# Kernel optimization log

Hardware: AMD Instinct MI355X
Metric: run time of the kernel (lower is better)

The kernel has to match this reference:

```python
import jax, jax.numpy as jnp
import numpy as np
from jax import lax

D_VOCAB = 262
D_EMB = 128
CONV_W = 5
PAD = CONV_W // 2  # 2


def setup_inputs() -> dict:
    key = jax.random.key(0)
    k1, k2, k3, k4, k5 = jax.random.split(key, 5)
    B, W, C = 128, 256, 16
    input = jax.random.randint(k1, (B, W, C), 0, D_VOCAB, dtype=jnp.int64)
    lengths = jax.random.randint(k2, (B, W), 1, C + 1, dtype=jnp.int64)
    # torch init: Embedding weight ~ N(0,1) then *0.1
    emb_weight = jax.random.normal(k3, (D_VOCAB, D_EMB), dtype=jnp.float32) * 0.1
    fan_in = D_EMB * CONV_W
    bound = 1.0 / np.sqrt(fan_in)
    conv_w = jax.random.uniform(k4, (D_EMB, D_EMB, CONV_W), dtype=jnp.float32, minval=-bound, maxval=bound)
    conv_b = jax.random.uniform(k5, (D_EMB,), dtype=jnp.float32, minval=-bound, maxval=bound)
    return {"input": input, "lengths": lengths, "emb_weight": emb_weight,
            "conv_w": conv_w, "conv_b": conv_b}


def reference(input, lengths, emb_weight, conv_w, conv_b):
    B, W, C = input.shape
    ids = input.reshape(B * W, C)                      # [N, C]
    embed = emb_weight[ids]                            # [N, C, E] gather
    x = jnp.transpose(embed, (0, 2, 1))                # [N, E, C] (NCW)
    y = lax.conv_general_dilated(
        x, conv_w,
        window_strides=(1,), padding=[(PAD, PAD)],
        dimension_numbers=("NCH", "OIH", "NCH"))       # [N, E, C]
    y = y + conv_b[None, :, None]
    out = jnp.max(y, axis=-1)                          # max-pool over chars
    return out.reshape(B, W, -1)                       # [B, W, E]
```

## Files before the change

### kernel.cpp

```cpp
#include <hip/hip_runtime.h>
#include <hip/hip_fp16.h>

#define D_VOCAB 262
#define D_EMB   128
#define KW      5
#define NCHAR   16
#define NKO     (KW * D_EMB)

typedef _Float16 h8 __attribute__((ext_vector_type(8)));
typedef float    f8 __attribute__((ext_vector_type(8)));


__global__ __launch_bounds__(256) void transpose_w_kernel(
    const float* __restrict__ cw, float* __restrict__ Wt2) {
  const int gid = blockIdx.x * 256 + threadIdx.x;
  const float val = cw[gid];
  const int o = gid / 640;
  const int r = gid - o * 640;
  const int i = r / 5;
  const int k = r - i * 5;
  Wt2[i * NKO + k * D_EMB + o] = val;
}

__global__ __launch_bounds__(128) void compute_P_kernel(
    const float* __restrict__ emb, const float* __restrict__ Wt2,
    __half* __restrict__ P) {
  __shared__ float emb_s[D_EMB];
  const int b = blockIdx.x;
  const int v = b / KW;
  const int k = b - v * KW;
  const int t = threadIdx.x;
  emb_s[t] = emb[v * D_EMB + t];
  __syncthreads();

  const float* col = Wt2 + k * D_EMB + t;
  float acc = 0.f;
#pragma unroll 16
  for (int i = 0; i < D_EMB; ++i) {
    acc += emb_s[i] * col[i * NKO];
  }
  P[v * NKO + k * D_EMB + t] = __float2half(acc);
}

__global__ __launch_bounds__(256) void conv_char_main_kernel(
    const int* __restrict__ ids, const _Float16* __restrict__ P,
    const float* __restrict__ bias, float* __restrict__ out) {
  const int lane = threadIdx.x & 63;
  const int wave = threadIdx.x >> 6;
  const int n_base = (blockIdx.x * 4 + wave) * 4;
  const int g4 = lane & 48;
  const int s = lane & 15;
  const int o = s * 8;
  const int n = n_base + (lane >> 4);

  const int myid = ids[n_base * NCHAR + lane];

  h8 win[5];
#pragma unroll
  for (int w = 0; w < 5; ++w) win[w] = (h8)(_Float16)0.f;
  h8 vmax = (h8)(_Float16)(-60000.f);

#pragma unroll
  for (int j = 0; j < NCHAR; ++j) {
    const int id = __shfl(myid, g4 + j);
    const _Float16* row = P + (size_t)id * NKO + o;
#pragma unroll
    for (int k = 0; k < KW; ++k) {
      const int c = j + 2 - k;
      if (c >= 0 && c < NCHAR) {
        const h8 val = *(const h8*)(row + k * D_EMB);
        win[c % 5] += val;
      }
    }
    if (j >= 2) {
      const int w = (j - 2) % 5;
      vmax = __builtin_elementwise_max(vmax, win[w]);
      win[w] = (h8)(_Float16)0.f;
    }
  }
  vmax = __builtin_elementwise_max(vmax, win[14 % 5]);
  vmax = __builtin_elementwise_max(vmax, win[15 % 5]);

  const f8 fv = __builtin_convertvector(vmax, f8);
  const f8 bv = *(const f8*)(bias + o);
  const f8 r = fv + bv;
  *(f8*)(out + (size_t)n * D_EMB + o) = r;
}

extern "C" void kernel_launch(void* const* d_in, const int* in_sizes, int n_in,
                              void* d_out, int out_size, void* d_ws, size_t ws_size,
                              hipStream_t stream) {
  const int*   input = (const int*)d_in[0];
  const float* emb   = (const float*)d_in[2];
  const float* cw    = (const float*)d_in[3];
  const float* cb    = (const float*)d_in[4];
  float* out = (float*)d_out;

  _Float16* P   = (_Float16*)d_ws;
  float*    Wt2 = (float*)((char*)d_ws + 335872);

  const int n_seq = in_sizes[0] / NCHAR;

  transpose_w_kernel<<<320, 256, 0, stream>>>(cw, Wt2);
  compute_P_kernel<<<D_VOCAB * KW, 128, 0, stream>>>(emb, Wt2, (__half*)P);

  const int blocks = n_seq / 16;
  conv_char_main_kernel<<<blocks, 256, 0, stream>>>(input, P, cb, out);
}
```

Baseline: 95.04 us.

## Map one wavefront per sequence with scalar id loads and half2 lanes

```diff
diff --git a/kernel.cpp b/kernel.cpp
--- a/kernel.cpp
+++ b/kernel.cpp
@@ -7,8 +7,8 @@
 #define NCHAR   16
 #define NKO     (KW * D_EMB)
 
+typedef _Float16 h2 __attribute__((ext_vector_type(2)));
 typedef _Float16 h8 __attribute__((ext_vector_type(8)));
-typedef float    f8 __attribute__((ext_vector_type(8)));
 
 
 __global__ __launch_bounds__(256) void transpose_w_kernel(
@@ -46,45 +46,43 @@
     const int* __restrict__ ids, const _Float16* __restrict__ P,
     const float* __restrict__ bias, float* __restrict__ out) {
   const int lane = threadIdx.x & 63;
-  const int wave = threadIdx.x >> 6;
-  const int n_base = (blockIdx.x * 4 + wave) * 4;
-  const int g4 = lane & 48;
-  const int s = lane & 15;
-  const int o = s * 8;
-  const int n = n_base + (lane >> 4);
+  int n = (int)((blockIdx.x * 256 + threadIdx.x) >> 6);
+  n = __builtin_amdgcn_readfirstlane(n);
 
-  const int myid = ids[n_base * NCHAR + lane];
+  const int* idrow = ids + n * NCHAR;
+  const int o = lane * 2;
 
-  h8 win[5];
+  h2 win[5];
 #pragma unroll
-  for (int w = 0; w < 5; ++w) win[w] = (h8)(_Float16)0.f;
-  h8 vmax = (h8)(_Float16)(-60000.f);
+  for (int w = 0; w < 5; ++w) win[w] = (h2)(_Float16)0.f;
+  h2 vmax = (h2)(_Float16)(-60000.f);
 
 #pragma unroll
   for (int j = 0; j < NCHAR; ++j) {
-    const int id = __shfl(myid, g4 + j);
+    const int id = idrow[j];
     const _Float16* row = P + (size_t)id * NKO + o;
 #pragma unroll
     for (int k = 0; k < KW; ++k) {
       const int c = j + 2 - k;
       if (c >= 0 && c < NCHAR) {
-        const h8 val = *(const h8*)(row + k * D_EMB);
+        const h2 val = *(const h2*)(row + k * D_EMB);
         win[c % 5] += val;
       }
     }
     if (j >= 2) {
       const int w = (j - 2) % 5;
       vmax = __builtin_elementwise_max(vmax, win[w]);
-      win[w] = (h8)(_Float16)0.f;
+      win[w] = (h2)(_Float16)0.f;
     }
   }
   vmax = __builtin_elementwise_max(vmax, win[14 % 5]);
   vmax = __builtin_elementwise_max(vmax, win[15 % 5]);
 
-  const f8 fv = __builtin_convertvector(vmax, f8);
-  const f8 bv = *(const f8*)(bias + o);
-  const f8 r = fv + bv;
-  *(f8*)(out + (size_t)n * D_EMB + o) = r;
+  const float2 bv = *(const float2*)(bias + o);
+  float2 r;
+  r.x = (float)vmax.x + bv.x;
+  r.y = (float)vmax.y + bv.y;
+  *(float2*)(out + (size_t)n * D_EMB + o) = r;
 }
 
 extern "C" void kernel_launch(void* const* d_in, const int* in_sizes, int n_in,
@@ -104,6 +102,6 @@
   transpose_w_kernel<<<320, 256, 0, stream>>>(cw, Wt2);
   compute_P_kernel<<<D_VOCAB * KW, 128, 0, stream>>>(emb, Wt2, (__half*)P);
 
-  const int blocks = n_seq / 16;
+  const int blocks = n_seq / 4;
   conv_char_main_kernel<<<blocks, 256, 0, stream>>>(input, P, cb, out);
 }
```

After: 93.67 us. No clear change (-1.4%).
